# Kernel optimization log

Hardware: AMD Instinct MI355X
Metric: run time of the kernel (lower is better)

Reference implementation:

```python
import jax, jax.numpy as jnp
import numpy as np

B, C, H, W = 8, 256, 64, 64
HEADS, R, TOPK_FRAC = 8, 4, 0.25
DIM = C // HEADS
SCALE = DIM ** -0.5


def setup_inputs() -> dict:
    key = jax.random.key(0)
    ks = jax.random.split(key, 8)
    s = 0.05
    return {
        "x": jax.random.normal(ks[0], (B, C, H, W), jnp.float32),
        "w_q": jax.random.normal(ks[1], (C, C), jnp.float32) * s,
        "w_k": jax.random.normal(ks[2], (C, C), jnp.float32) * s,
        "w_v": jax.random.normal(ks[3], (C, C), jnp.float32) * s,
        "w_ck": jax.random.normal(ks[4], (C, R, R), jnp.float32) * s,  # depthwise kxk
        "w_cv": jax.random.normal(ks[5], (C, R, R), jnp.float32) * s,
        "w_out": jax.random.normal(ks[6], (C, C), jnp.float32) * s,
        "b_out": jax.random.normal(ks[7], (C,), jnp.float32) * s,
    }


def _conv1x1(x, w):
    # x: [B,C,H,W], w: [O,C]
    return jnp.einsum('bchw,oc->bohw', x, w)


def _depthwise_pool(x, w):
    # depthwise conv, kernel=stride=R -> non-overlapping blocks
    b, c, h, wd = x.shape
    blocks = x.reshape(b, c, h // R, R, wd // R, R)
    return jnp.einsum('bcirjs,crs->bcij', blocks, w)


def reference(x, w_q, w_k, w_v, w_ck, w_cv, w_out, b_out):
    N = H * W
    q = _conv1x1(x, w_q)
    k = _conv1x1(x, w_k)
    v = _conv1x1(x, w_v)
    k_s = _depthwise_pool(k, w_ck)   # [B,C,H/R,W/R]
    v_s = _depthwise_pool(v, w_cv)
    n = k_s.shape[2] * k_s.shape[3]

    BH = B * HEADS
    q = q.reshape(B, HEADS, DIM, N).reshape(BH, DIM, N)
    k = k_s.reshape(B, HEADS, DIM, n).reshape(BH, DIM, n)
    v = v_s.reshape(B, HEADS, DIM, n).reshape(BH, DIM, n)

    # stage 1: full queries vs compressed keys
    attn = jax.nn.softmax(jnp.einsum('bdi,bdj->bij', q, k) * SCALE, axis=-1)
    token_score = attn.sum(axis=1)                     # [BH, n]
    top_k = max(1, int(n * TOPK_FRAC))
    _, idx = jax.lax.top_k(token_score, top_k)         # [BH, top_k]

    idx_exp = jnp.broadcast_to(idx[:, None, :], (BH, DIM, top_k))
    k_top = jnp.take_along_axis(k, idx_exp, axis=2)    # [BH, DIM, top_k]
    v_top = jnp.take_along_axis(v, idx_exp, axis=2)

    # stage 2: attend only to selected compressed tokens
    attn_full = jax.nn.softmax(jnp.einsum('bdi,bdj->bij', q, k_top) * SCALE, axis=-1)
    out = jnp.einsum('bij,bdj->bdi', attn_full, v_top)  # [BH, DIM, N]
    out = out.reshape(B, HEADS, DIM, N).reshape(B, C, H, W)
    return _conv1x1(out, w_out) + b_out[None, :, None, None]
```

## Files before the change

kernel.cpp:

```cpp
#include <hip/hip_runtime.h>

#define Bq 8
#define Cq 256
#define Hq 64
#define Wq 64
#define Nq 4096
#define HEADSq 8
#define DIMq 32
#define NCq 256
#define TOPKq 64
#define BHq 64
#define SCALEq 0.17677669529663687f

typedef short bf16x8 __attribute__((ext_vector_type(8)));
typedef float f32x16 __attribute__((ext_vector_type(16)));

__device__ __forceinline__ uint32_t f2bf_hi(float f) {
  uint32_t u = __float_as_uint(f);
  return (u + 0x7FFFu + ((u >> 16) & 1u)) >> 16;
}

__device__ __forceinline__ void split8(const float* v, uint4& hv, uint4& lv) {
  uint32_t h[8], l[8];
#pragma unroll
  for (int j = 0; j < 8; ++j) {
    uint32_t hb = f2bf_hi(v[j]);
    float rest = v[j] - __uint_as_float(hb << 16);
    h[j] = hb;
    l[j] = __float_as_uint(rest) >> 16;
  }
  hv = make_uint4(h[0] | (h[1] << 16), h[2] | (h[3] << 16),
                  h[4] | (h[5] << 16), h[6] | (h[7] << 16));
  lv = make_uint4(l[0] | (l[1] << 16), l[2] | (l[3] << 16),
                  l[4] | (l[5] << 16), l[6] | (l[7] << 16));
}


__global__ __launch_bounds__(256) void prep_w(
    const float* __restrict__ wq, const float* __restrict__ wk,
    const float* __restrict__ wv, const float* __restrict__ wo,
    char* __restrict__ wt) {
  const int oblk = blockIdx.x, s = blockIdx.y, mat = blockIdx.z;
  const float* w = mat == 0 ? wq : mat == 1 ? wk : mat == 2 ? wv : wo;
  const int t = threadIdx.x;
  const int o = t & 63, g = t >> 6;
  float v[8];
  const float* src = w + (size_t)(oblk * 64 + o) * Cq + s * 32 + g * 8;
#pragma unroll
  for (int j = 0; j < 8; ++j) v[j] = src[j];
  uint4 hv, lv;
  split8(v, hv, lv);
  size_t base = ((size_t)((mat * 4 + oblk) * 8 + s)) * 8192;
  int off = ((o >> 5) * 2 + (g >> 1)) * 1024 + ((o & 31) + 32 * (g & 1)) * 16;
  *(uint4*)(wt + base + off) = hv;
  *(uint4*)(wt + base + 4096 + off) = lv;
}

__global__ __launch_bounds__(256) void qkv_mfma(
    const float* __restrict__ x, const char* __restrict__ wt,
    float* __restrict__ q, float* __restrict__ kf, float* __restrict__ vf) {
  const int b = blockIdx.z, oblk = blockIdx.y, nblk = blockIdx.x;
  const int o0 = oblk * 64, n0 = nblk * 64;
  const int t = threadIdx.x, l = t & 63, wid = t >> 6;
  const int ob = wid >> 1, nbw = wid & 1;
  __shared__ __align__(16) short wimg[3][2][2048];
  __shared__ __align__(16) short ximg[2][2048];
  __shared__ __align__(16) float xf[32][64];
  f32x16 acc[3];
#pragma unroll
  for (int m = 0; m < 3; ++m)
#pragma unroll
    for (int i = 0; i < 16; ++i) acc[m][i] = 0.f;

  for (int s = 0; s < 8; ++s) {
    __syncthreads();
#pragma unroll
    for (int i = 0; i < 6; ++i) {
      const int m = i >> 1;
      const int off = t + (i & 1) * 256;
      ((uint4*)&wimg[m][0][0])[off] =
          ((const uint4*)(wt + ((size_t)((m * 4 + oblk) * 8 + s)) * 8192))[off];
    }
    {
      const float* xb = x + ((size_t)(b * Cq + s * 32)) * Nq + n0;
#pragma unroll
      for (int i = 0; i < 2; ++i) {
        int e = t + i * 256;
        int cl = e >> 4, n4 = (e & 15) * 4;
        *(float4*)&xf[cl][n4] = *(const float4*)&xb[(size_t)cl * Nq + n4];
      }
    }
    __syncthreads();
    {
      int n = t & 63, g = t >> 6;
      float v[8];
#pragma unroll
      for (int j = 0; j < 8; ++j) v[j] = xf[g * 8 + j][n];
      uint4 hv, lv;
      split8(v, hv, lv);
      int off = ((n >> 5) * 2 + (g >> 1)) * 1024 + ((n & 31) + 32 * (g & 1)) * 16;
      *(uint4*)((char*)&ximg[0][0] + off) = hv;
      *(uint4*)((char*)&ximg[1][0] + off) = lv;
    }
    __syncthreads();
    bf16x8 bh[2], bl[2];
#pragma unroll
    for (int kh = 0; kh < 2; ++kh) {
      int off = (nbw * 2 + kh) * 1024 + l * 16;
      bh[kh] = *(const bf16x8*)((const char*)&ximg[0][0] + off);
      bl[kh] = *(const bf16x8*)((const char*)&ximg[1][0] + off);
    }
#pragma unroll
    for (int m = 0; m < 3; ++m) {
#pragma unroll
      for (int kh = 0; kh < 2; ++kh) {
        int off = (ob * 2 + kh) * 1024 + l * 16;
        bf16x8 ah = *(const bf16x8*)((const char*)&wimg[m][0][0] + off);
        bf16x8 al = *(const bf16x8*)((const char*)&wimg[m][1][0] + off);
        acc[m] = __builtin_amdgcn_mfma_f32_32x32x16_bf16(ah, bh[kh], acc[m], 0, 0, 0);
        acc[m] = __builtin_amdgcn_mfma_f32_32x32x16_bf16(ah, bl[kh], acc[m], 0, 0, 0);
        acc[m] = __builtin_amdgcn_mfma_f32_32x32x16_bf16(al, bh[kh], acc[m], 0, 0, 0);
      }
    }
  }
#pragma unroll
  for (int m = 0; m < 3; ++m) {
    float* dst = (m == 0 ? q : m == 1 ? kf : vf) + (size_t)b * Cq * Nq;
#pragma unroll
    for (int r = 0; r < 16; ++r) {
      int orow = o0 + ob * 32 + (r & 3) + 8 * (r >> 2) + 4 * (l >> 5);
      dst[(size_t)orow * Nq + n0 + nbw * 32 + (l & 31)] = acc[m][r];
    }
  }
}

__global__ __launch_bounds__(256) void pool_kv(
    const float* __restrict__ kf, const float* __restrict__ vf,
    const float* __restrict__ wck, const float* __restrict__ wcv,
    float* __restrict__ ks, float* __restrict__ vs) {
  int bc = blockIdx.x;
  int b = bc / Cq, c = bc % Cq;
  int t = threadIdx.x;
  int i = t >> 4, j = t & 15;
  const float* kp = kf + ((size_t)b * Cq + c) * Nq;
  const float* vp = vf + ((size_t)b * Cq + c) * Nq;
  __shared__ float wk_s[16], wv_s[16];
  if (t < 16) { wk_s[t] = wck[c * 16 + t]; wv_s[t] = wcv[c * 16 + t]; }
  __syncthreads();
  float ak = 0.f, av = 0.f;
#pragma unroll
  for (int r = 0; r < 4; ++r)
#pragma unroll
    for (int s = 0; s < 4; ++s) {
      int n = (i * 4 + r) * Wq + j * 4 + s;
      float wkv = wk_s[r * 4 + s], wvv = wv_s[r * 4 + s];
      ak += kp[n] * wkv;
      av += vp[n] * wvv;
    }
  ks[((size_t)b * Cq + c) * NCq + t] = ak;
  vs[((size_t)b * Cq + c) * NCq + t] = av;
}

__global__ __launch_bounds__(256, 2) void stage1_mfma(
    const float* __restrict__ q, const float* __restrict__ ks,
    float* __restrict__ part) {
  const int bh = blockIdx.y, b = bh >> 3, h = bh & 7;
  const int row0 = blockIdx.x * 512;
  const int t = threadIdx.x, l = t & 63, wid = t >> 6;
  __shared__ __align__(16) short kimg[2][4][2048];
  __shared__ __align__(16) short qimg[2][2][2048];
  __shared__ __align__(16) float xf[32][128];
  __shared__ float sc[4][256];

  const float* qb = q + ((size_t)b * Cq + h * DIMq) * Nq;
  const float* kb = ks + ((size_t)b * Cq + h * DIMq) * NCq;

#pragma unroll
  for (int half = 0; half < 2; ++half) {
    __syncthreads();
#pragma unroll
    for (int i = 0; i < 4; ++i) {
      int row = (t >> 5) + i * 8, c4 = (t & 31) * 4;
      *(float4*)&xf[row][c4] =
          *(const float4*)&kb[(size_t)row * NCq + half * 128 + c4];
    }
    __syncthreads();
#pragma unroll
    for (int i = 0; i < 2; ++i) {
      int e = t + i * 256;
      int n = e & 127, g = e >> 7;
      float v[8];
#pragma unroll
      for (int j = 0; j < 8; ++j) v[j] = xf[g * 8 + j][n];
      uint4 hv, lv;
      split8(v, hv, lv);
      int img = half * 2 + (n >> 6), row = n & 63;
      int off = ((row >> 5) * 2 + (g >> 1)) * 1024 +
                ((row & 31) + 32 * (g & 1)) * 16;
      *(uint4*)((char*)&kimg[0][img][0] + off) = hv;
      *(uint4*)((char*)&kimg[1][img][0] + off) = lv;
    }
  }

  float scoreacc[8];
#pragma unroll
  for (int g = 0; g < 8; ++g) scoreacc[g] = 0.f;

  for (int step = 0; step < 4; ++step) {
    const int r0 = row0 + step * 128;
    __syncthreads();
#pragma unroll
    for (int i = 0; i < 4; ++i) {
      int row = (t >> 5) + i * 8, c4 = (t & 31) * 4;
      *(float4*)&xf[row][c4] = *(const float4*)&qb[(size_t)row * Nq + r0 + c4];
    }
    __syncthreads();
#pragma unroll
    for (int i = 0; i < 2; ++i) {
      int e = t + i * 256;
      int n = e & 127, g = e >> 7;
      float v[8];
#pragma unroll
      for (int j = 0; j < 8; ++j) v[j] = xf[g * 8 + j][n];
      uint4 hv, lv;
      split8(v, hv, lv);
      int img = n >> 6, row = n & 63;
      int off = ((row >> 5) * 2 + (g >> 1)) * 1024 +
                ((row & 31) + 32 * (g & 1)) * 16;
      *(uint4*)((char*)&qimg[0][img][0] + off) = hv;
      *(uint4*)((char*)&qimg[1][img][0] + off) = lv;
    }
    __syncthreads();
    bf16x8 ah[2], al[2];
#pragma unroll
    for (int kh = 0; kh < 2; ++kh) {
      int off = ((wid & 1) * 2 + kh) * 1024 + l * 16;
      ah[kh] = *(const bf16x8*)((const char*)&qimg[0][wid >> 1][0] + off);
      al[kh] = *(const bf16x8*)((const char*)&qimg[1][wid >> 1][0] + off);
    }
    f32x16 acc[8];
#pragma unroll
    for (int g = 0; g < 8; ++g)
#pragma unroll
      for (int r = 0; r < 16; ++r) acc[g][r] = 0.f;
#pragma unroll
    for (int img = 0; img < 4; ++img)
#pragma unroll
      for (int nb = 0; nb < 2; ++nb) {
        const int g = img * 2 + nb;
#pragma unroll
        for (int kh = 0; kh < 2; ++kh) {
          int off = (nb * 2 + kh) * 1024 + l * 16;
          bf16x8 bh = *(const bf16x8*)((const char*)&kimg[0][img][0] + off);
          bf16x8 bl = *(const bf16x8*)((const char*)&kimg[1][img][0] + off);
          acc[g] = __builtin_amdgcn_mfma_f32_32x32x16_bf16(ah[kh], bh, acc[g], 0, 0, 0);
          acc[g] = __builtin_amdgcn_mfma_f32_32x32x16_bf16(ah[kh], bl, acc[g], 0, 0, 0);
          acc[g] = __builtin_amdgcn_mfma_f32_32x32x16_bf16(al[kh], bh, acc[g], 0, 0, 0);
        }
      }
    float mx[16], sm[16];
#pragma unroll
    for (int r = 0; r < 16; ++r) {
      float m = acc[0][r];
#pragma unroll
      for (int g = 1; g < 8; ++g) m = fmaxf(m, acc[g][r]);
      mx[r] = m;
    }
#pragma unroll
    for (int off = 1; off < 32; off <<= 1)
#pragma unroll
      for (int r = 0; r < 16; ++r) mx[r] = fmaxf(mx[r], __shfl_xor(mx[r], off));
#pragma unroll
    for (int r = 0; r < 16; ++r) sm[r] = 0.f;
#pragma unroll
    for (int g = 0; g < 8; ++g)
#pragma unroll
      for (int r = 0; r < 16; ++r) {
        float e = __expf((acc[g][r] - mx[r]) * SCALEq);
        acc[g][r] = e;
        sm[r] += e;
      }
#pragma unroll
    for (int off = 1; off < 32; off <<= 1)
#pragma unroll
      for (int r = 0; r < 16; ++r) sm[r] += __shfl_xor(sm[r], off);
#pragma unroll
    for (int r = 0; r < 16; ++r) sm[r] = 1.0f / sm[r];
#pragma unroll
    for (int g = 0; g < 8; ++g) {
      float tp = 0.f;
#pragma unroll
      for (int r = 0; r < 16; ++r) tp += acc[g][r] * sm[r];
      tp += __shfl_xor(tp, 32);
      scoreacc[g] += tp;
    }
  }
  if (l < 32) {
#pragma unroll
    for (int g = 0; g < 8; ++g) sc[wid][g * 32 + l] = scoreacc[g];
  }
  __syncthreads();
  {
    float v = sc[0][t] + sc[1][t] + sc[2][t] + sc[3][t];
    part[((size_t)bh * 8 + blockIdx.x) * NCq + t] = v;
  }
}

__global__ __launch_bounds__(256) void reduce_scores(
    const float* __restrict__ part, float* __restrict__ score) {
  int bh = blockIdx.x, t = threadIdx.x;
  float s = 0.f;
#pragma unroll
  for (int c = 0; c < 8; ++c) s += part[((size_t)bh * 8 + c) * NCq + t];
  score[bh * NCq + t] = s;
}

__global__ __launch_bounds__(256) void topk_sel(
    const float* __restrict__ score, int* __restrict__ idx) {
  int bh = blockIdx.x, t = threadIdx.x;
  __shared__ float s[NCq];
  s[t] = score[bh * NCq + t];
  __syncthreads();
  float st = s[t];
  int rank = 0;
  for (int j = 0; j < NCq; ++j) {
    float sj = s[j];
    rank += (sj > st) || (sj == st && j < t);
  }
  if (rank < TOPKq) idx[bh * TOPKq + rank] = t;
}

__global__ __launch_bounds__(256) void stage2_attn(
    const float* __restrict__ q, const float* __restrict__ ks,
    const float* __restrict__ vs, const int* __restrict__ idx,
    char* __restrict__ at) {
  const int bh = blockIdx.y, b = bh >> 3, h = bh & 7;
  const int nb = blockIdx.x;
  const int n0 = nb * 64;
  const int t = threadIdx.x;
  __shared__ float kt[DIMq][TOPKq];
  __shared__ float vt[DIMq][TOPKq];
  __shared__ float qs[DIMq][64];
  __shared__ float L[64][TOPKq + 1];
  const float* ksb = ks + ((size_t)b * Cq + h * DIMq) * NCq;
  const float* vsb = vs + ((size_t)b * Cq + h * DIMq) * NCq;
  const int* ib = idx + bh * TOPKq;
  for (int e = t; e < DIMq * TOPKq; e += 256) {
    int d = e >> 6, j = e & 63;
    int tok = ib[j];
    kt[d][j] = ksb[(size_t)d * NCq + tok];
    vt[d][j] = vsb[(size_t)d * NCq + tok];
  }
  const float* qb = q + ((size_t)b * Cq + h * DIMq) * Nq;
  for (int e = t; e < DIMq * 64; e += 256) {
    int d = e >> 6, r = e & 63;
    qs[d][r] = qb[(size_t)d * Nq + n0 + r];
  }
  __syncthreads();
  {
    int r = t & 63;
    int tg = (t >> 6) * 16;
    float acc[16];
#pragma unroll
    for (int j = 0; j < 16; ++j) acc[j] = 0.f;
    for (int d = 0; d < DIMq; ++d) {
      float qd = qs[d][r];
#pragma unroll
      for (int j = 0; j < 16; ++j) acc[j] += qd * kt[d][tg + j];
    }
#pragma unroll
    for (int j = 0; j < 16; ++j) L[r][tg + j] = acc[j] * SCALEq;
  }
  __syncthreads();
  if (t < 64) {
    float m = -1e30f;
    for (int j = 0; j < TOPKq; ++j) m = fmaxf(m, L[t][j]);
    float s = 0.f;
    for (int j = 0; j < TOPKq; ++j) { float e = __expf(L[t][j] - m); L[t][j] = e; s += e; }
    float inv = 1.0f / s;
    for (int j = 0; j < TOPKq; ++j) L[t][j] *= inv;
  }
  __syncthreads();
  {
    int r = t & 63;
    int d0 = (t >> 6) * 8;
    float acc[8] = {};
    for (int j = 0; j < TOPKq; ++j) {
      float a = L[r][j];
#pragma unroll
      for (int dd = 0; dd < 8; ++dd) acc[dd] += a * vt[d0 + dd][j];
    }
    uint4 hv, lv;
    split8(acc, hv, lv);
    size_t base = ((size_t)((b * 64 + nb) * 8 + h)) * 8192;
    int off = ((r >> 5) * 2 + (d0 >> 4)) * 1024 +
              ((r & 31) + 32 * ((d0 >> 3) & 1)) * 16;
    *(uint4*)(at + base + off) = hv;
    *(uint4*)(at + base + 4096 + off) = lv;
  }
}

__global__ __launch_bounds__(256) void out_mfma(
    const char* __restrict__ at, const char* __restrict__ wt,
    const float* __restrict__ bo, float* __restrict__ y) {
  const int b = blockIdx.z, oblk = blockIdx.y, nblk = blockIdx.x;
  const int o0 = oblk * 64, n0 = nblk * 64;
  const int t = threadIdx.x, l = t & 63, wid = t >> 6;
  const int ob = wid >> 1, nbw = wid & 1;
  __shared__ __align__(16) short wimg[2][2048];
  __shared__ __align__(16) short ximg[2][2048];
  __shared__ float bs[64];
  if (t < 64) bs[t] = bo[o0 + t];
  f32x16 acc;
#pragma unroll
  for (int i = 0; i < 16; ++i) acc[i] = 0.f;

  for (int s = 0; s < 8; ++s) {
    __syncthreads();
    {
      const uint4* srcw = (const uint4*)(wt + ((size_t)((12 + oblk) * 8 + s)) * 8192);
      const uint4* srcx = (const uint4*)(at + ((size_t)((b * 64 + nblk) * 8 + s)) * 8192);
#pragma unroll
      for (int i = 0; i < 2; ++i) {
        ((uint4*)&wimg[0][0])[t + i * 256] = srcw[t + i * 256];
        ((uint4*)&ximg[0][0])[t + i * 256] = srcx[t + i * 256];
      }
    }
    __syncthreads();
#pragma unroll
    for (int kh = 0; kh < 2; ++kh) {
      int offa = (ob * 2 + kh) * 1024 + l * 16;
      int offb = (nbw * 2 + kh) * 1024 + l * 16;
      bf16x8 ah = *(const bf16x8*)((const char*)&wimg[0][0] + offa);
      bf16x8 al = *(const bf16x8*)((const char*)&wimg[1][0] + offa);
      bf16x8 bh = *(const bf16x8*)((const char*)&ximg[0][0] + offb);
      bf16x8 bl = *(const bf16x8*)((const char*)&ximg[1][0] + offb);
      acc = __builtin_amdgcn_mfma_f32_32x32x16_bf16(ah, bh, acc, 0, 0, 0);
      acc = __builtin_amdgcn_mfma_f32_32x32x16_bf16(ah, bl, acc, 0, 0, 0);
      acc = __builtin_amdgcn_mfma_f32_32x32x16_bf16(al, bh, acc, 0, 0, 0);
    }
  }
#pragma unroll
  for (int r = 0; r < 16; ++r) {
    int ol = ob * 32 + (r & 3) + 8 * (r >> 2) + 4 * (l >> 5);
    y[((size_t)(b * Cq + o0 + ol)) * Nq + n0 + nbw * 32 + (l & 31)] = acc[r] + bs[ol];
  }
}

extern "C" void kernel_launch(void* const* d_in, const int* in_sizes, int n_in,
                              void* d_out, int out_size, void* d_ws, size_t ws_size,
                              hipStream_t stream) {
  const float* x   = (const float*)d_in[0];
  const float* wq  = (const float*)d_in[1];
  const float* wk  = (const float*)d_in[2];
  const float* wv  = (const float*)d_in[3];
  const float* wck = (const float*)d_in[4];
  const float* wcv = (const float*)d_in[5];
  const float* wo  = (const float*)d_in[6];
  const float* bo  = (const float*)d_in[7];
  float* out = (float*)d_out;

  float* ws = (float*)d_ws;
  const size_t SZ_FULL = (size_t)Bq * Cq * Nq;
  const size_t SZ_CMP  = (size_t)Bq * Cq * NCq;
  float* q     = ws;
  float* kf    = q  + SZ_FULL;
  float* vf    = kf + SZ_FULL;
  float* ksc   = vf + SZ_FULL;
  float* vsc   = ksc + SZ_CMP;
  float* part  = vsc + SZ_CMP;
  float* score = part + (size_t)BHq * 8 * NCq;
  int*   idx   = (int*)(score + (size_t)BHq * NCq);
  char*  wt    = (char*)(idx + (size_t)BHq * TOPKq);
  char*  at    = (char*)kf;

  prep_w<<<dim3(4, 8, 4), 256, 0, stream>>>(wq, wk, wv, wo, wt);
  qkv_mfma<<<dim3(64, 4, 8), 256, 0, stream>>>(x, wt, q, kf, vf);
  pool_kv<<<dim3(Bq * Cq), 256, 0, stream>>>(kf, vf, wck, wcv, ksc, vsc);
  stage1_mfma<<<dim3(8, BHq), 256, 0, stream>>>(q, ksc, part);
  reduce_scores<<<dim3(BHq), 256, 0, stream>>>(part, score);
  topk_sel<<<dim3(BHq), 256, 0, stream>>>(score, idx);
  stage2_attn<<<dim3(64, BHq), 256, 0, stream>>>(q, ksc, vsc, idx, at);
  out_mfma<<<dim3(64, 4, 8), 256, 0, stream>>>(at, wt, bo, out);
}
```

Before: 216.3 us.

## Rewrite stage-2 attention with split-bf16 MFMA and in-register softmax

Replaces the scalar FP32 stage-2 attention kernel with one that uses 32x32x16 bf16 MFMA for both QK^T and PV. Precision is kept near FP32 by splitting each value into hi/lo bf16 parts and issuing three MFMAs per product. The softmax now runs across lanes with shuffles instead of 64 threads looping serially. Each block handles 128 query rows instead of 64, which halves the grid, and the kernel adds a launch_bounds occupancy hint. The cost is extra split/convert work and LDS staging, plus a small precision loss from dropping the lo*lo term.

```diff
diff --git a/kernel.cpp b/kernel.cpp
--- a/kernel.cpp
+++ b/kernel.cpp
@@ -330,71 +330,159 @@
   if (rank < TOPKq) idx[bh * TOPKq + rank] = t;
 }
 
-__global__ __launch_bounds__(256) void stage2_attn(
+__global__ __launch_bounds__(256, 2) void stage2_mfma(
     const float* __restrict__ q, const float* __restrict__ ks,
     const float* __restrict__ vs, const int* __restrict__ idx,
     char* __restrict__ at) {
   const int bh = blockIdx.y, b = bh >> 3, h = bh & 7;
-  const int nb = blockIdx.x;
-  const int n0 = nb * 64;
-  const int t = threadIdx.x;
-  __shared__ float kt[DIMq][TOPKq];
-  __shared__ float vt[DIMq][TOPKq];
-  __shared__ float qs[DIMq][64];
-  __shared__ float L[64][TOPKq + 1];
+  const int n0 = blockIdx.x * 128;
+  const int t = threadIdx.x, l = t & 63, wid = t >> 6;
+  __shared__ __align__(16) short kimg[2][2048];
+  __shared__ __align__(16) short vimg[2][2][1024];
+  __shared__ __align__(16) short qimg[2][2][2048];
+  __shared__ float pbuf[128][66];
+  __shared__ int ibs[64];
+
+  const float* qb = q + ((size_t)b * Cq + h * DIMq) * Nq;
   const float* ksb = ks + ((size_t)b * Cq + h * DIMq) * NCq;
   const float* vsb = vs + ((size_t)b * Cq + h * DIMq) * NCq;
-  const int* ib = idx + bh * TOPKq;
-  for (int e = t; e < DIMq * TOPKq; e += 256) {
-    int d = e >> 6, j = e & 63;
-    int tok = ib[j];
-    kt[d][j] = ksb[(size_t)d * NCq + tok];
-    vt[d][j] = vsb[(size_t)d * NCq + tok];
-  }
-  const float* qb = q + ((size_t)b * Cq + h * DIMq) * Nq;
-  for (int e = t; e < DIMq * 64; e += 256) {
-    int d = e >> 6, r = e & 63;
-    qs[d][r] = qb[(size_t)d * Nq + n0 + r];
-  }
-  __syncthreads();
+  if (t < 64) ibs[t] = idx[bh * TOPKq + t];
+  __syncthreads();
+
   {
-    int r = t & 63;
-    int tg = (t >> 6) * 16;
-    float acc[16];
-#pragma unroll
-    for (int j = 0; j < 16; ++j) acc[j] = 0.f;
-    for (int d = 0; d < DIMq; ++d) {
-      float qd = qs[d][r];
-#pragma unroll
-      for (int j = 0; j < 16; ++j) acc[j] += qd * kt[d][tg + j];
-    }
-#pragma unroll
-    for (int j = 0; j < 16; ++j) L[r][tg + j] = acc[j] * SCALEq;
-  }
-  __syncthreads();
-  if (t < 64) {
-    float m = -1e30f;
-    for (int j = 0; j < TOPKq; ++j) m = fmaxf(m, L[t][j]);
-    float s = 0.f;
-    for (int j = 0; j < TOPKq; ++j) { float e = __expf(L[t][j] - m); L[t][j] = e; s += e; }
-    float inv = 1.0f / s;
-    for (int j = 0; j < TOPKq; ++j) L[t][j] *= inv;
-  }
-  __syncthreads();
+    int tok = t & 63, dg = t >> 6;
+    int ti = ibs[tok];
+    float v[8];
+#pragma unroll
+    for (int j = 0; j < 8; ++j) v[j] = ksb[(size_t)(dg * 8 + j) * NCq + ti];
+    uint4 hv, lv;
+    split8(v, hv, lv);
+    int off = ((tok >> 5) * 2 + (dg >> 1)) * 1024 + ((tok & 31) + 32 * (dg & 1)) * 16;
+    *(uint4*)((char*)&kimg[0][0] + off) = hv;
+    *(uint4*)((char*)&kimg[1][0] + off) = lv;
+  }
   {
-    int r = t & 63;
-    int d0 = (t >> 6) * 8;
-    float acc[8] = {};
-    for (int j = 0; j < TOPKq; ++j) {
-      float a = L[r][j];
-#pragma unroll
-      for (int dd = 0; dd < 8; ++dd) acc[dd] += a * vt[d0 + dd][j];
+    int d = l & 31, tko = l >> 5, img = (t >> 6) >> 1, kreg = (t >> 6) & 1;
+    float v[8];
+#pragma unroll
+    for (int j = 0; j < 8; ++j) {
+      int tok = img * 32 + kreg * 16 + tko * 8 + j;
+      v[j] = vsb[(size_t)d * NCq + ibs[tok]];
     }
     uint4 hv, lv;
-    split8(acc, hv, lv);
+    split8(v, hv, lv);
+    int off = kreg * 1024 + (d + 32 * tko) * 16;
+    *(uint4*)((char*)&vimg[0][img][0] + off) = hv;
+    *(uint4*)((char*)&vimg[1][img][0] + off) = lv;
+  }
+#pragma unroll
+  for (int qi = 0; qi < 2; ++qi) {
+    int qr = t & 63, dg = t >> 6;
+    float v[8];
+#pragma unroll
+    for (int j = 0; j < 8; ++j)
+      v[j] = qb[(size_t)(dg * 8 + j) * Nq + n0 + qi * 64 + qr];
+    uint4 hv, lv;
+    split8(v, hv, lv);
+    int off = ((qr >> 5) * 2 + (dg >> 1)) * 1024 + ((qr & 31) + 32 * (dg & 1)) * 16;
+    *(uint4*)((char*)&qimg[0][qi][0] + off) = hv;
+    *(uint4*)((char*)&qimg[1][qi][0] + off) = lv;
+  }
+  __syncthreads();
+
+  f32x16 pacc[2];
+#pragma unroll
+  for (int g = 0; g < 2; ++g)
+#pragma unroll
+    for (int r = 0; r < 16; ++r) pacc[g][r] = 0.f;
+  {
+    bf16x8 ah[2], al[2];
+#pragma unroll
+    for (int kd = 0; kd < 2; ++kd) {
+      int off = ((wid & 1) * 2 + kd) * 1024 + l * 16;
+      ah[kd] = *(const bf16x8*)((const char*)&qimg[0][wid >> 1][0] + off);
+      al[kd] = *(const bf16x8*)((const char*)&qimg[1][wid >> 1][0] + off);
+    }
+#pragma unroll
+    for (int g = 0; g < 2; ++g)
+#pragma unroll
+      for (int kd = 0; kd < 2; ++kd) {
+        int off = (g * 2 + kd) * 1024 + l * 16;
+        bf16x8 bh = *(const bf16x8*)((const char*)&kimg[0][0] + off);
+        bf16x8 bl = *(const bf16x8*)((const char*)&kimg[1][0] + off);
+        pacc[g] = __builtin_amdgcn_mfma_f32_32x32x16_bf16(ah[kd], bh, pacc[g], 0, 0, 0);
+        pacc[g] = __builtin_amdgcn_mfma_f32_32x32x16_bf16(ah[kd], bl, pacc[g], 0, 0, 0);
+        pacc[g] = __builtin_amdgcn_mfma_f32_32x32x16_bf16(al[kd], bh, pacc[g], 0, 0, 0);
+      }
+  }
+  {
+    float mx[16], sm[16];
+#pragma unroll
+    for (int r = 0; r < 16; ++r) mx[r] = fmaxf(pacc[0][r], pacc[1][r]);
+#pragma unroll
+    for (int off = 1; off < 32; off <<= 1)
+#pragma unroll
+      for (int r = 0; r < 16; ++r) mx[r] = fmaxf(mx[r], __shfl_xor(mx[r], off));
+#pragma unroll
+    for (int r = 0; r < 16; ++r) {
+      float e0 = __expf((pacc[0][r] - mx[r]) * SCALEq);
+      float e1 = __expf((pacc[1][r] - mx[r]) * SCALEq);
+      pacc[0][r] = e0; pacc[1][r] = e1;
+      sm[r] = e0 + e1;
+    }
+#pragma unroll
+    for (int off = 1; off < 32; off <<= 1)
+#pragma unroll
+      for (int r = 0; r < 16; ++r) sm[r] += __shfl_xor(sm[r], off);
+#pragma unroll
+    for (int r = 0; r < 16; ++r) sm[r] = 1.0f / sm[r];
+#pragma unroll
+    for (int g = 0; g < 2; ++g)
+#pragma unroll
+      for (int r = 0; r < 16; ++r) {
+        int qrow = wid * 32 + (r & 3) + 8 * (r >> 2) + 4 * (l >> 5);
+        pbuf[qrow][g * 32 + (l & 31)] = pacc[g][r] * sm[r];
+      }
+  }
+  __syncthreads();
+  f32x16 oacc;
+#pragma unroll
+  for (int r = 0; r < 16; ++r) oacc[r] = 0.f;
+#pragma unroll
+  for (int ks4 = 0; ks4 < 4; ++ks4) {
+    const float* pa = &pbuf[wid * 32 + (l & 31)][ks4 * 16 + (l >> 5) * 8];
+    float v[8];
+#pragma unroll
+    for (int j = 0; j < 8; ++j) v[j] = pa[j];
+    uint4 hv, lv;
+    split8(v, hv, lv);
+    bf16x8 pah = *(const bf16x8*)&hv, pal = *(const bf16x8*)&lv;
+    int off = (ks4 & 1) * 1024 + l * 16;
+    bf16x8 bh = *(const bf16x8*)((const char*)&vimg[0][ks4 >> 1][0] + off);
+    bf16x8 bl = *(const bf16x8*)((const char*)&vimg[1][ks4 >> 1][0] + off);
+    oacc = __builtin_amdgcn_mfma_f32_32x32x16_bf16(pah, bh, oacc, 0, 0, 0);
+    oacc = __builtin_amdgcn_mfma_f32_32x32x16_bf16(pah, bl, oacc, 0, 0, 0);
+    oacc = __builtin_amdgcn_mfma_f32_32x32x16_bf16(pal, bh, oacc, 0, 0, 0);
+  }
+#pragma unroll
+  for (int r = 0; r < 16; ++r) {
+    int qrow = wid * 32 + (r & 3) + 8 * (r >> 2) + 4 * (l >> 5);
+    pbuf[qrow][l & 31] = oacc[r];
+  }
+  __syncthreads();
+#pragma unroll
+  for (int i = 0; i < 2; ++i) {
+    int slot = t + i * 256;
+    int row = slot >> 2, dg = slot & 3;
+    float v[8];
+#pragma unroll
+    for (int j = 0; j < 8; ++j) v[j] = pbuf[row][dg * 8 + j];
+    uint4 hv, lv;
+    split8(v, hv, lv);
+    int nb = blockIdx.x * 2 + (row >> 6), nloc = row & 63;
     size_t base = ((size_t)((b * 64 + nb) * 8 + h)) * 8192;
-    int off = ((r >> 5) * 2 + (d0 >> 4)) * 1024 +
-              ((r & 31) + 32 * ((d0 >> 3) & 1)) * 16;
+    int off = ((nloc >> 5) * 2 + (dg >> 1)) * 1024 +
+              ((nloc & 31) + 32 * (dg & 1)) * 16;
     *(uint4*)(at + base + off) = hv;
     *(uint4*)(at + base + 4096 + off) = lv;
   }
@@ -480,6 +568,6 @@
   stage1_mfma<<<dim3(8, BHq), 256, 0, stream>>>(q, ksc, part);
   reduce_scores<<<dim3(BHq), 256, 0, stream>>>(part, score);
   topk_sel<<<dim3(BHq), 256, 0, stream>>>(score, idx);
-  stage2_attn<<<dim3(64, BHq), 256, 0, stream>>>(q, ksc, vsc, idx, at);
+  stage2_mfma<<<dim3(32, BHq), 256, 0, stream>>>(q, ksc, vsc, idx, at);
   out_mfma<<<dim3(64, 4, 8), 256, 0, stream>>>(at, wt, bo, out);
 }
```

After: 185.3 us. 1.17x faster.
